# Kernel optimization log

Measured on AMD Instinct MI355X. Metric: run time of the kernel, lower is better.

The kernel has to match this reference:

```python
import jax, jax.numpy as jnp
import numpy as np

N_NODES = 100000
N_EDGES = 1600000
D_IN = 128
D_HID = 128
D_OUT = 128


def setup_inputs() -> dict:
    key = jax.random.key(0)
    ks = jax.random.split(key, 8)
    s = lambda d: 1.0 / np.sqrt(d)
    return {
        "x": jax.random.normal(ks[0], (N_NODES, D_IN), dtype=jnp.float32),
        "edge_src": jax.random.randint(ks[1], (N_EDGES,), 0, N_NODES, dtype=jnp.int64),
        "edge_dst": jax.random.randint(ks[2], (N_EDGES,), 0, N_NODES, dtype=jnp.int64),
        "W1": jax.random.normal(ks[3], (D_IN, D_HID), dtype=jnp.float32) * s(D_IN),
        "b1": jnp.zeros((D_HID,), dtype=jnp.float32),
        "W_self": jax.random.normal(ks[4], (D_HID, D_HID), dtype=jnp.float32) * s(D_HID),
        "W_neigh": jax.random.normal(ks[5], (D_HID, D_HID), dtype=jnp.float32) * s(D_HID),
        "b_sage": jnp.zeros((D_HID,), dtype=jnp.float32),
        "W2": jax.random.normal(ks[6], (D_HID, D_OUT), dtype=jnp.float32) * s(D_HID),
        "b2": jnp.zeros((D_OUT,), dtype=jnp.float32),
    }


def reference(x, edge_src, edge_dst, W1, b1, W_self, W_neigh, b_sage, W2, b2):
    n_dst = x.shape[0]
    # d1: Linear + ReLU  [N, D_IN] -> [N, D_HID]
    h = jax.nn.relu(x @ W1 + b1)
    # SAGEConv 'mean': gather src features per edge, mean-reduce per dst node
    msg = h[edge_src]  # [E, D_HID] irregular gather
    neigh_sum = jax.ops.segment_sum(msg, edge_dst, num_segments=n_dst)
    deg = jax.ops.segment_sum(jnp.ones((edge_dst.shape[0],), h.dtype), edge_dst, num_segments=n_dst)
    h_neigh = neigh_sum / jnp.maximum(deg, 1.0)[:, None]
    # fc_self(h_dst) + fc_neigh(h_neigh) + bias, then activation (relu)
    h2 = jax.nn.relu(h @ W_self + h_neigh @ W_neigh + b_sage)
    # d2: Linear + ReLU
    return jax.nn.relu(h2 @ W2 + b2)
```

## Files before the change

### kernel.cpp

```cpp
#include <hip/hip_runtime.h>


typedef __bf16 bf16x8 __attribute__((ext_vector_type(8)));
typedef float f32x4 __attribute__((ext_vector_type(4)));
typedef float f32x2 __attribute__((ext_vector_type(2)));

#define D 128
#define SRC_BITS 17
#define OCT_SH 14
#define OCT_CAP 270336
#define BCAP 1536
#define BINCHUNK 4096

__device__ __forceinline__ unsigned short f2bf(float f){
  unsigned int u = __float_as_uint(f);
  u += 0x7FFF + ((u >> 16) & 1);
  return (unsigned short)(u >> 16);
}

__global__ void prep_w_all(const float* __restrict__ Wa, const float* __restrict__ Wb,
                           const float* __restrict__ Wc, const float* __restrict__ Wd,
                           unsigned short* __restrict__ Ta, unsigned short* __restrict__ Tb,
                           unsigned short* __restrict__ Tc, unsigned short* __restrict__ Td){
  int which = blockIdx.x >> 7;
  int k = blockIdx.x & 127;
  int n = threadIdx.x;
  const float* W = (which == 0) ? Wa : (which == 1) ? Wb : (which == 2) ? Wc : Wd;
  unsigned short* T = (which == 0) ? Ta : (which == 1) ? Tb : (which == 2) ? Tc : Td;
  T[n * D + k] = f2bf(W[k * D + n]);
}

__launch_bounds__(256, 4)
__global__ void gemm1_bin8(const float* __restrict__ A,
                           const unsigned short* __restrict__ Wt,
                           const float* __restrict__ bias,
                           unsigned short* __restrict__ hout,
                           unsigned char* __restrict__ h8out,
                           const int* __restrict__ esrc, const int* __restrict__ edst,
                           int* __restrict__ ofill, unsigned* __restrict__ eoct,
                           int M, int E, int nblk, int nchunk)
{
  __shared__ unsigned short As[128 * 128];
  const int t = threadIdx.x;
  const int lane = t & 63;
  const int bid = blockIdx.x;
  const int g = bid >> 1, r = bid & 1;

  if (r == 1){
    const int chunk = g;
    if (chunk >= nchunk) return;
    int* lcnt  = (int*)As;
    int* lbase = (int*)As + 16;
    int* lrank = (int*)As + 32;
    if (t < 8){ lcnt[t] = 0; lrank[t] = 0; }
    __syncthreads();
    const int base = chunk * BINCHUNK;
    const int lim = min(base + BINCHUNK, E);

    int myc = 0;
    for (int i0 = base + (t >> 6) * 64; i0 < lim; i0 += 256){
      int i = i0 + lane;
      int o = (i < lim) ? (edst[i] >> OCT_SH) : 8;
      #pragma unroll
      for (int k = 0; k < 8; k++){
        unsigned long long bk = __ballot(o == k);
        if (lane == k) myc += (int)__popcll(bk);
      }
    }
    if (lane < 8 && myc) atomicAdd(&lcnt[lane], myc);
    __syncthreads();
    if (t < 8) lbase[t] = atomicAdd(&ofill[t * 16], lcnt[t]);
    __syncthreads();

    for (int i0 = base + (t >> 6) * 64; i0 < lim; i0 += 256){
      int i = i0 + lane;
      bool valid = i < lim;
      int s = 0, o = 8, dloc = 0;
      if (valid){
        int d = edst[i];
        s = esrc[i];
        o = d >> OCT_SH;
        dloc = d & ((1 << OCT_SH) - 1);
      }
      int rank = 0, wcnt = 0;
      #pragma unroll
      for (int k = 0; k < 8; k++){
        unsigned long long bk = __ballot(o == k);
        if (o == k) rank = (int)__popcll(bk & ((1ull << lane) - 1));
        if (lane == k) wcnt = (int)__popcll(bk);
      }
      int wv = 0;
      if (lane < 8) wv = atomicAdd(&lrank[lane], wcnt);
      int mybase = __shfl(wv, o & 7);
      if (valid){
        int p = lbase[o] + mybase + rank;
        if (p < OCT_CAP)
          eoct[(size_t)o * OCT_CAP + p] = (unsigned)s | ((unsigned)dloc << SRC_BITS);
      }
    }
    return;
  }

  if (g >= nblk) return;
  const int wave = t >> 6;
  const int rowBase = g * 128;

  f32x4 zero = {0.f, 0.f, 0.f, 0.f};
  f32x4 acc[4][4];
  #pragma unroll
  for (int i = 0; i < 4; i++)
    #pragma unroll
    for (int j = 0; j < 4; j++) acc[i][j] = zero;

  #pragma unroll
  for (int i = 0; i < 8; i++){
    int idx = t + i * 256;
    int row = idx >> 4;
    int inb = (idx & 15) << 4;
    int gg = rowBase + row; if (gg >= M) gg = M - 1;
    const float* src = A + (size_t)gg * D + (inb >> 1);
    float4 v0 = *(const float4*)src;
    float4 v1 = *(const float4*)(src + 4);
    uint4 o;
    o.x = (unsigned)f2bf(v0.x) | ((unsigned)f2bf(v0.y) << 16);
    o.y = (unsigned)f2bf(v0.z) | ((unsigned)f2bf(v0.w) << 16);
    o.z = (unsigned)f2bf(v1.x) | ((unsigned)f2bf(v1.y) << 16);
    o.w = (unsigned)f2bf(v1.z) | ((unsigned)f2bf(v1.w) << 16);
    *(uint4*)((char*)As + row * 256 + (inb ^ ((row & 7) << 4))) = o;
  }
  __syncthreads();

  const int wr = (wave >> 1) * 64;
  const int wc = (wave & 1) * 64;
  const int fr = lane & 15;
  const int kg = lane >> 4;

  #pragma unroll
  for (int ks = 0; ks < 4; ks++){
    int kb = ks * 64 + kg * 16;
    bf16x8 a[4], b[4];
    #pragma unroll
    for (int mi = 0; mi < 4; mi++){
      int row = wr + mi * 16 + fr;
      a[mi] = __builtin_bit_cast(bf16x8, *(const uint4*)((const char*)As + row * 256 + (kb ^ ((row & 7) << 4))));
    }
    #pragma unroll
    for (int ni = 0; ni < 4; ni++){
      int row = wc + ni * 16 + fr;
      b[ni] = __builtin_bit_cast(bf16x8, *(const uint4*)((const char*)Wt + row * 256 + kb));
    }
    #pragma unroll
    for (int mi = 0; mi < 4; mi++)
      #pragma unroll
      for (int ni = 0; ni < 4; ni++)
        acc[mi][ni] = __builtin_amdgcn_mfma_f32_16x16x32_bf16(a[mi], b[ni], acc[mi][ni], 0, 0, 0);
  }

  #pragma unroll
  for (int ni = 0; ni < 4; ni++){
    int col = wc + ni * 16 + fr;
    float bv = bias[col];
    #pragma unroll
    for (int mi = 0; mi < 4; mi++)
      #pragma unroll
      for (int j = 0; j < 4; j++){
        int row = rowBase + wr + mi * 16 + kg * 4 + j;
        if (row < M){
          float v = fmaxf(acc[mi][ni][j] + bv, 0.0f);
          hout[(size_t)row * D + col] = f2bf(v);
          int p8 = __builtin_amdgcn_cvt_pk_fp8_f32(v, v, 0, false);
          h8out[(size_t)row * D + col] = (unsigned char)(p8 & 0xff);
        }
      }
  }
}

__launch_bounds__(256)
__global__ void bin_bucket(const unsigned* __restrict__ eoct, const int* __restrict__ ofill,
                           int* __restrict__ bfill, unsigned* __restrict__ ebkt){
  __shared__ int lcnt[256], lbase[256], lpos[256];
  const int o = blockIdx.x & 7;
  const int chunk = blockIdx.x >> 3;
  const int n = min(ofill[o * 16], OCT_CAP);
  const int base = chunk * 2048;
  if (base >= n) return;
  const int lim = min(base + 2048, n);
  const unsigned* lst = eoct + (size_t)o * OCT_CAP;
  const int t = threadIdx.x;
  lcnt[t] = 0;
  __syncthreads();
  for (int i = base + t; i < lim; i += 256){
    int dloc = (int)(lst[i] >> SRC_BITS);
    atomicAdd(&lcnt[dloc >> 6], 1);
  }
  __syncthreads();
  if (lcnt[t] > 0) lbase[t] = atomicAdd(&bfill[((o << 8) + t) * 16], lcnt[t]);
  lpos[t] = 0;
  __syncthreads();
  for (int i = base + t; i < lim; i += 256){
    unsigned w = lst[i];
    int dloc = (int)(w >> SRC_BITS);
    int bk = dloc >> 6;
    int r = atomicAdd(&lpos[bk], 1);
    int p = lbase[bk] + r;
    unsigned v = (w & ((1u << SRC_BITS) - 1)) | ((unsigned)(dloc & 63) << SRC_BITS);
    if (p < BCAP) ebkt[(size_t)((o << 8) + bk) * BCAP + p] = v;
  }
}

__launch_bounds__(512)
__global__ void gather_sorted(const unsigned char* __restrict__ h8,
                              const unsigned* __restrict__ ebkt,
                              const int* __restrict__ bfill,
                              unsigned short* __restrict__ hn, int M){
  __shared__ unsigned earr[BCAP];
  __shared__ int lcnt[64], lbeg[64], lpos[64];
  const int b = blockIdx.x;
  const int t = threadIdx.x;
  const int lane = t & 63;
  const int wave = t >> 6;
  const int half = lane >> 5;
  const int li = lane & 31;
  const int nE = min(bfill[b * 16], BCAP);
  const int nodeBase = b << 6;
  const int nNodes = min(64, M - nodeBase);
  const unsigned* lst = ebkt + (size_t)b * BCAP;

  if (t < 64) lcnt[t] = 0;
  __syncthreads();
  for (int i = t; i < nE; i += 512)
    atomicAdd(&lcnt[lst[i] >> SRC_BITS], 1);
  __syncthreads();
  if (wave == 0){
    int c = lcnt[lane];
    int x = c;
    #pragma unroll
    for (int d = 1; d < 64; d <<= 1){
      int v = __shfl_up(x, d);
      if (lane >= d) x += v;
    }
    lbeg[lane] = x;
    lpos[lane] = x - c;
  }
  __syncthreads();
  for (int i = t; i < nE; i += 512){
    unsigned w = lst[i];
    int k = (int)(w >> SRC_BITS);
    int p = atomicAdd(&lpos[k], 1);
    earr[p] = (w & ((1u << SRC_BITS) - 1)) << 7;
  }
  __syncthreads();

  const int li4 = li * 4;
  for (int nI = wave; nI < nNodes; nI += 8){
    int deg = lcnt[nI];
    int end = lbeg[nI];
    int beg = end - deg;
    float a0 = 0.f, a1 = 0.f, a2 = 0.f, a3 = 0.f;
    int i = beg;
    for (; i + 16 <= end; i += 16){
      unsigned pk[8];
      #pragma unroll
      for (int u = 0; u < 8; u++)
        pk[u] = *(const unsigned*)(h8 + earr[i + 2 * u + half] + li4);
      #pragma unroll
      for (int u = 0; u < 8; u++){
        f32x2 f01 = __builtin_amdgcn_cvt_pk_f32_fp8(pk[u], false);
        f32x2 f23 = __builtin_amdgcn_cvt_pk_f32_fp8(pk[u], true);
        a0 += f01[0]; a1 += f01[1]; a2 += f23[0]; a3 += f23[1];
      }
    }
    for (; i + 2 <= end; i += 2){
      unsigned v = *(const unsigned*)(h8 + earr[i + half] + li4);
      f32x2 f01 = __builtin_amdgcn_cvt_pk_f32_fp8(v, false);
      f32x2 f23 = __builtin_amdgcn_cvt_pk_f32_fp8(v, true);
      a0 += f01[0]; a1 += f01[1]; a2 += f23[0]; a3 += f23[1];
    }
    if (i < end && half == 0){
      unsigned v = *(const unsigned*)(h8 + earr[i] + li4);
      f32x2 f01 = __builtin_amdgcn_cvt_pk_f32_fp8(v, false);
      f32x2 f23 = __builtin_amdgcn_cvt_pk_f32_fp8(v, true);
      a0 += f01[0]; a1 += f01[1]; a2 += f23[0]; a3 += f23[1];
    }
    a0 += __shfl_xor(a0, 32); a1 += __shfl_xor(a1, 32);
    a2 += __shfl_xor(a2, 32); a3 += __shfl_xor(a3, 32);
    if (half == 0){
      float inv = 1.0f / (float)max(deg, 1);
      uint2 ov;
      ov.x = (unsigned)f2bf(a0 * inv) | ((unsigned)f2bf(a1 * inv) << 16);
      ov.y = (unsigned)f2bf(a2 * inv) | ((unsigned)f2bf(a3 * inv) << 16);
      *(uint2*)(hn + (size_t)(nodeBase + nI) * D + li4) = ov;
    }
  }
}

#define STAGE_BF16(A, dstLDS)                                              \
  _Pragma("unroll")                                                        \
  for (int i = 0; i < 8; i++){                                             \
    int idx = t + i * 256;                                                 \
    int row = idx >> 4;                                                    \
    int inb = (idx & 15) << 4;                                             \
    int g = rowBase + row; if (g >= M) g = M - 1;                          \
    uint4 v = *(const uint4*)((const char*)(A) + (size_t)g * 256 + inb);   \
    *(uint4*)((char*)(dstLDS) + row * 256 + (inb ^ ((row & 7) << 4))) = v; \
  }

__launch_bounds__(256, 4)
__global__ void gemm_fused(const unsigned short* __restrict__ h,
                           const unsigned short* __restrict__ Wst,
                           const unsigned short* __restrict__ hn,
                           const unsigned short* __restrict__ Wnt,
                           const unsigned short* __restrict__ W2t,
                           const float* __restrict__ bsage,
                           const float* __restrict__ b2,
                           float* __restrict__ out, int M)
{
  __shared__ unsigned short As[128 * 128];
  const int t = threadIdx.x;
  const int lane = t & 63;
  const int wave = t >> 6;
  const int rowBase = blockIdx.x * 128;

  const int wr = (wave >> 1) * 64;
  const int wc = (wave & 1) * 64;
  const int fr = lane & 15;
  const int kg = lane >> 4;

  f32x4 zero = {0.f, 0.f, 0.f, 0.f};
  f32x4 acc[4][4];
  #pragma unroll
  for (int i = 0; i < 4; i++)
    #pragma unroll
    for (int j = 0; j < 4; j++) acc[i][j] = zero;

  auto mma_pass = [&](const unsigned short* W){
    #pragma unroll
    for (int ks = 0; ks < 4; ks++){
      int kb = ks * 64 + kg * 16;
      bf16x8 a[4], b[4];
      #pragma unroll
      for (int mi = 0; mi < 4; mi++){
        int row = wr + mi * 16 + fr;
        a[mi] = __builtin_bit_cast(bf16x8, *(const uint4*)((const char*)As + row * 256 + (kb ^ ((row & 7) << 4))));
      }
      #pragma unroll
      for (int ni = 0; ni < 4; ni++){
        int row = wc + ni * 16 + fr;
        b[ni] = __builtin_bit_cast(bf16x8, *(const uint4*)((const char*)W + row * 256 + kb));
      }
      #pragma unroll
      for (int mi = 0; mi < 4; mi++)
        #pragma unroll
        for (int ni = 0; ni < 4; ni++)
          acc[mi][ni] = __builtin_amdgcn_mfma_f32_16x16x32_bf16(a[mi], b[ni], acc[mi][ni], 0, 0, 0);
    }
  };

  uint4 hreg[8];
  #pragma unroll
  for (int i = 0; i < 8; i++){
    int idx = t + i * 256;
    int row = idx >> 4;
    int inb = (idx & 15) << 4;
    int g = rowBase + row; if (g >= M) g = M - 1;
    hreg[i] = *(const uint4*)((const char*)hn + (size_t)g * 256 + inb);
  }

  STAGE_BF16(h, As);
  __syncthreads();
  mma_pass(Wst);
  __syncthreads();

  #pragma unroll
  for (int i = 0; i < 8; i++){
    int idx = t + i * 256;
    int row = idx >> 4;
    int inb = (idx & 15) << 4;
    *(uint4*)((char*)As + row * 256 + (inb ^ ((row & 7) << 4))) = hreg[i];
  }
  __syncthreads();
  mma_pass(Wnt);
  __syncthreads();

  #pragma unroll
  for (int ni = 0; ni < 4; ni++){
    int col = wc + ni * 16 + fr;
    float bv = bsage[col];
    #pragma unroll
    for (int mi = 0; mi < 4; mi++)
      #pragma unroll
      for (int j = 0; j < 4; j++){
        int row = wr + mi * 16 + kg * 4 + j;
        unsigned short hv = f2bf(fmaxf(acc[mi][ni][j] + bv, 0.0f));
        *(unsigned short*)((char*)As + row * 256 + ((col * 2) ^ ((row & 7) << 4))) = hv;
        acc[mi][ni][j] = 0.f;
      }
  }
  __syncthreads();
  mma_pass(W2t);

  #pragma unroll
  for (int ni = 0; ni < 4; ni++){
    int col = wc + ni * 16 + fr;
    float bv = b2[col];
    #pragma unroll
    for (int mi = 0; mi < 4; mi++)
      #pragma unroll
      for (int j = 0; j < 4; j++){
        int row = rowBase + wr + mi * 16 + kg * 4 + j;
        if (row < M)
          out[(size_t)row * D + col] = fmaxf(acc[mi][ni][j] + bv, 0.0f);
      }
  }
}

extern "C" void kernel_launch(void* const* d_in, const int* in_sizes, int n_in,
                              void* d_out, int out_size, void* d_ws, size_t ws_size,
                              hipStream_t stream)
{
  const float* x     = (const float*)d_in[0];
  const int*   esrc  = (const int*)d_in[1];
  const int*   edst  = (const int*)d_in[2];
  const float* W1    = (const float*)d_in[3];
  const float* b1    = (const float*)d_in[4];
  const float* Wself = (const float*)d_in[5];
  const float* Wneigh= (const float*)d_in[6];
  const float* bsage = (const float*)d_in[7];
  const float* W2    = (const float*)d_in[8];
  const float* b2    = (const float*)d_in[9];

  const int M = in_sizes[0] / D;
  const int E = in_sizes[1];
  const int NBK = (M + 63) >> 6;

  char* ws = (char*)d_ws;
  unsigned short* W1t = (unsigned short*)(ws);
  unsigned short* Wst = (unsigned short*)(ws + 32768);
  unsigned short* Wnt = (unsigned short*)(ws + 65536);
  unsigned short* W2t = (unsigned short*)(ws + 98304);
  size_t hbytes = (size_t)M * D * 2;
  unsigned short* h   = (unsigned short*)(ws + 131072);
  unsigned short* hn  = (unsigned short*)(ws + 131072 + hbytes);
  unsigned char*  h8  = (unsigned char*)(ws + 131072 + 2 * hbytes);
  char* p = ws + 131072 + 2 * hbytes + (size_t)M * D;
  int* ofill = (int*)p;                  p += 8 * 16 * 4;
  int* bfill = (int*)p;                  p += (size_t)2048 * 16 * 4;
  unsigned* eoct = (unsigned*)p;         p += (size_t)8 * OCT_CAP * 4;
  unsigned* ebkt = (unsigned*)p;

  prep_w_all<<<4 * D, D, 0, stream>>>(W1, Wself, Wneigh, W2, W1t, Wst, Wnt, W2t);
  hipMemsetAsync(ofill, 0, 512 + (size_t)2048 * 16 * 4, stream);

  const int nblk = (M + 127) / 128;
  const int nchunk = (E + BINCHUNK - 1) / BINCHUNK;

  gemm1_bin8<<<2 * nblk, 256, 0, stream>>>(x, W1t, b1, h, h8, esrc, edst,
                                           ofill, eoct, M, E, nblk, nchunk);

  {
    int chunks = (OCT_CAP + 2047) / 2048;
    bin_bucket<<<8 * chunks, 256, 0, stream>>>(eoct, ofill, bfill, ebkt);
  }

  gather_sorted<<<NBK, 512, 0, stream>>>(h8, ebkt, bfill, hn, M);

  gemm_fused<<<nblk, 256, 0, stream>>>(h, Wst, hn, Wnt, W2t, bsage, b2, (float*)d_out, M);
}
```

Before: 174.9 us.

## Move GEMM1 overlap from octant binning to bucket binning stage

Splits the first edge-binning pass (by destination octant) into its own kernel. The first GEMM is then co-scheduled with the second binning pass (bucket scatter), interleaving 3 GEMM tiles and 4 bucket chunks per group of 7 blocks. The aim is to hide the bucket-scatter kernel's latency behind the dense GEMM instead of hiding the octant pass. This removes one serial launch boundary but reshuffles which work overlaps. The grid mapping must cover every GEMM tile and bucket chunk: 264 groups × 3 = 792 ≥ 782 tiles and 264 × 4 = 1056 = nbchunk.

```diff
diff --git a/kernel.cpp b/kernel.cpp
--- a/kernel.cpp
+++ b/kernel.cpp
@@ -30,80 +30,115 @@
   T[n * D + k] = f2bf(W[k * D + n]);
 }
 
+__launch_bounds__(256)
+__global__ void bin8(const int* __restrict__ esrc, const int* __restrict__ edst,
+                     int* __restrict__ ofill, unsigned* __restrict__ eoct, int E){
+  __shared__ int lcnt[8], lbase[8], lrank[8];
+  const int t = threadIdx.x;
+  const int lane = t & 63;
+  if (t < 8){ lcnt[t] = 0; lrank[t] = 0; }
+  __syncthreads();
+  const int base = blockIdx.x * BINCHUNK;
+  const int lim = min(base + BINCHUNK, E);
+
+  int myc = 0;
+  for (int i0 = base + (t >> 6) * 64; i0 < lim; i0 += 256){
+    int i = i0 + lane;
+    int o = (i < lim) ? (edst[i] >> OCT_SH) : 8;
+    #pragma unroll
+    for (int k = 0; k < 8; k++){
+      unsigned long long bk = __ballot(o == k);
+      if (lane == k) myc += (int)__popcll(bk);
+    }
+  }
+  if (lane < 8 && myc) atomicAdd(&lcnt[lane], myc);
+  __syncthreads();
+  if (t < 8) lbase[t] = atomicAdd(&ofill[t * 16], lcnt[t]);
+  __syncthreads();
+
+  for (int i0 = base + (t >> 6) * 64; i0 < lim; i0 += 256){
+    int i = i0 + lane;
+    bool valid = i < lim;
+    int s = 0, o = 8, dloc = 0;
+    if (valid){
+      int d = edst[i];
+      s = esrc[i];
+      o = d >> OCT_SH;
+      dloc = d & ((1 << OCT_SH) - 1);
+    }
+    int rank = 0, wcnt = 0;
+    #pragma unroll
+    for (int k = 0; k < 8; k++){
+      unsigned long long bk = __ballot(o == k);
+      if (o == k) rank = (int)__popcll(bk & ((1ull << lane) - 1));
+      if (lane == k) wcnt = (int)__popcll(bk);
+    }
+    int wv = 0;
+    if (lane < 8) wv = atomicAdd(&lrank[lane], wcnt);
+    int mybase = __shfl(wv, o & 7);
+    if (valid){
+      int p = lbase[o] + mybase + rank;
+      if (p < OCT_CAP)
+        eoct[(size_t)o * OCT_CAP + p] = (unsigned)s | ((unsigned)dloc << SRC_BITS);
+    }
+  }
+}
+
 __launch_bounds__(256, 4)
-__global__ void gemm1_bin8(const float* __restrict__ A,
-                           const unsigned short* __restrict__ Wt,
-                           const float* __restrict__ bias,
-                           unsigned short* __restrict__ hout,
-                           unsigned char* __restrict__ h8out,
-                           const int* __restrict__ esrc, const int* __restrict__ edst,
-                           int* __restrict__ ofill, unsigned* __restrict__ eoct,
-                           int M, int E, int nblk, int nchunk)
+__global__ void gemm1_bucket(const float* __restrict__ A,
+                             const unsigned short* __restrict__ Wt,
+                             const float* __restrict__ bias,
+                             unsigned short* __restrict__ hout,
+                             unsigned char* __restrict__ h8out,
+                             const unsigned* __restrict__ eoct, const int* __restrict__ ofill,
+                             int* __restrict__ bfill, unsigned* __restrict__ ebkt,
+                             int M, int nblk, int nbchunk)
 {
   __shared__ unsigned short As[128 * 128];
   const int t = threadIdx.x;
   const int lane = t & 63;
   const int bid = blockIdx.x;
-  const int g = bid >> 1, r = bid & 1;
-
-  if (r == 1){
-    const int chunk = g;
-    if (chunk >= nchunk) return;
+  const int g = bid / 7, r = bid % 7;
+
+  if (r >= 3){
+    const int c = g * 4 + (r - 3);
+    if (c >= nbchunk) return;
+    const int o = c & 7;
+    const int chunk = c >> 3;
+    const int n = min(ofill[o * 16], OCT_CAP);
+    const int base = chunk * 2048;
+    if (base >= n) return;
+    const int lim = min(base + 2048, n);
+    const unsigned* lst = eoct + (size_t)o * OCT_CAP;
     int* lcnt  = (int*)As;
-    int* lbase = (int*)As + 16;
-    int* lrank = (int*)As + 32;
-    if (t < 8){ lcnt[t] = 0; lrank[t] = 0; }
+    int* lbase = (int*)As + 256;
+    int* lpos  = (int*)As + 512;
+    lcnt[t] = 0;
     __syncthreads();
-    const int base = chunk * BINCHUNK;
-    const int lim = min(base + BINCHUNK, E);
-
-    int myc = 0;
-    for (int i0 = base + (t >> 6) * 64; i0 < lim; i0 += 256){
-      int i = i0 + lane;
-      int o = (i < lim) ? (edst[i] >> OCT_SH) : 8;
-      #pragma unroll
-      for (int k = 0; k < 8; k++){
-        unsigned long long bk = __ballot(o == k);
-        if (lane == k) myc += (int)__popcll(bk);
-      }
-    }
-    if (lane < 8 && myc) atomicAdd(&lcnt[lane], myc);
+    for (int i = base + t; i < lim; i += 256){
+      int dloc = (int)(lst[i] >> SRC_BITS);
+      atomicAdd(&lcnt[dloc >> 6], 1);
+    }
     __syncthreads();
-    if (t < 8) lbase[t] = atomicAdd(&ofill[t * 16], lcnt[t]);
+    if (lcnt[t] > 0) lbase[t] = atomicAdd(&bfill[((o << 8) + t) * 16], lcnt[t]);
+    lpos[t] = 0;
     __syncthreads();
-
-    for (int i0 = base + (t >> 6) * 64; i0 < lim; i0 += 256){
-      int i = i0 + lane;
-      bool valid = i < lim;
-      int s = 0, o = 8, dloc = 0;
-      if (valid){
-        int d = edst[i];
-        s = esrc[i];
-        o = d >> OCT_SH;
-        dloc = d & ((1 << OCT_SH) - 1);
-      }
-      int rank = 0, wcnt = 0;
-      #pragma unroll
-      for (int k = 0; k < 8; k++){
-        unsigned long long bk = __ballot(o == k);
-        if (o == k) rank = (int)__popcll(bk & ((1ull << lane) - 1));
-        if (lane == k) wcnt = (int)__popcll(bk);
-      }
-      int wv = 0;
-      if (lane < 8) wv = atomicAdd(&lrank[lane], wcnt);
-      int mybase = __shfl(wv, o & 7);
-      if (valid){
-        int p = lbase[o] + mybase + rank;
-        if (p < OCT_CAP)
-          eoct[(size_t)o * OCT_CAP + p] = (unsigned)s | ((unsigned)dloc << SRC_BITS);
-      }
+    for (int i = base + t; i < lim; i += 256){
+      unsigned w = lst[i];
+      int dloc = (int)(w >> SRC_BITS);
+      int bk = dloc >> 6;
+      int rr = atomicAdd(&lpos[bk], 1);
+      int p = lbase[bk] + rr;
+      unsigned v = (w & ((1u << SRC_BITS) - 1)) | ((unsigned)(dloc & 63) << SRC_BITS);
+      if (p < BCAP) ebkt[(size_t)((o << 8) + bk) * BCAP + p] = v;
     }
     return;
   }
 
-  if (g >= nblk) return;
+  const int tile = g * 3 + r;
+  if (tile >= nblk) return;
   const int wave = t >> 6;
-  const int rowBase = g * 128;
+  const int rowBase = tile * 128;
 
   f32x4 zero = {0.f, 0.f, 0.f, 0.f};
   f32x4 acc[4][4];
@@ -172,39 +207,6 @@
           h8out[(size_t)row * D + col] = (unsigned char)(p8 & 0xff);
         }
       }
-  }
-}
-
-__launch_bounds__(256)
-__global__ void bin_bucket(const unsigned* __restrict__ eoct, const int* __restrict__ ofill,
-                           int* __restrict__ bfill, unsigned* __restrict__ ebkt){
-  __shared__ int lcnt[256], lbase[256], lpos[256];
-  const int o = blockIdx.x & 7;
-  const int chunk = blockIdx.x >> 3;
-  const int n = min(ofill[o * 16], OCT_CAP);
-  const int base = chunk * 2048;
-  if (base >= n) return;
-  const int lim = min(base + 2048, n);
-  const unsigned* lst = eoct + (size_t)o * OCT_CAP;
-  const int t = threadIdx.x;
-  lcnt[t] = 0;
-  __syncthreads();
-  for (int i = base + t; i < lim; i += 256){
-    int dloc = (int)(lst[i] >> SRC_BITS);
-    atomicAdd(&lcnt[dloc >> 6], 1);
-  }
-  __syncthreads();
-  if (lcnt[t] > 0) lbase[t] = atomicAdd(&bfill[((o << 8) + t) * 16], lcnt[t]);
-  lpos[t] = 0;
-  __syncthreads();
-  for (int i = base + t; i < lim; i += 256){
-    unsigned w = lst[i];
-    int dloc = (int)(w >> SRC_BITS);
-    int bk = dloc >> 6;
-    int r = atomicAdd(&lpos[bk], 1);
-    int p = lbase[bk] + r;
-    unsigned v = (w & ((1u << SRC_BITS) - 1)) | ((unsigned)(dloc & 63) << SRC_BITS);
-    if (p < BCAP) ebkt[(size_t)((o << 8) + bk) * BCAP + p] = v;
   }
 }
 
@@ -453,13 +455,15 @@
 
   const int nblk = (M + 127) / 128;
   const int nchunk = (E + BINCHUNK - 1) / BINCHUNK;
-
-  gemm1_bin8<<<2 * nblk, 256, 0, stream>>>(x, W1t, b1, h, h8, esrc, edst,
-                                           ofill, eoct, M, E, nblk, nchunk);
+  const int nbchunk = 8 * ((OCT_CAP + 2047) / 2048);
+
+  bin8<<<nchunk, 256, 0, stream>>>(esrc, edst, ofill, eoct, E);
 
   {
-    int chunks = (OCT_CAP + 2047) / 2048;
-    bin_bucket<<<8 * chunks, 256, 0, stream>>>(eoct, ofill, bfill, ebkt);
+    int ngroups = 264;
+    gemm1_bucket<<<7 * ngroups, 256, 0, stream>>>(x, W1t, b1, h, h8,
+                                                  eoct, ofill, bfill, ebkt,
+                                                  M, nblk, nbchunk);
   }
 
   gather_sorted<<<NBK, 512, 0, stream>>>(h8, ebkt, bfill, hn, M);
```

New measurement: 175.9 us. About the same (+0.6%).
